# Kernel optimization log

Hardware: AMD Instinct MI355X
Metric: run time of the kernel (lower is better)

The kernel has to match this reference:

```python
import jax, jax.numpy as jnp
import numpy as np

NEG_INF = -jnp.inf


def setup_inputs() -> dict:
    key = jax.random.key(0)
    ks = jax.random.split(key, 8)
    B, Lq, Lk, D, H = 8, 2048, 2048, 256, 128
    queries = jax.random.normal(ks[0], (B, Lq, D), dtype=jnp.float32)
    keys = jax.random.normal(ks[1], (B, Lk, D), dtype=jnp.float32)
    values_1 = jax.random.normal(ks[2], (B, Lk, D), dtype=jnp.float32)
    values_2 = jax.random.normal(ks[3], (B, Lq, D), dtype=jnp.float32)
    values_1_mask = jax.random.randint(ks[4], (B, Lk), 0, 2).astype(bool)
    values_2_mask = jax.random.randint(ks[5], (B, Lq), 0, 2).astype(bool)
    # xavier_normal for Linear(D -> H): std = sqrt(2/(D+H))
    std = float(np.sqrt(2.0 / (D + H)))
    Wq = jax.random.normal(ks[6], (H, D), dtype=jnp.float32) * std
    Wk = jax.random.normal(ks[7], (H, D), dtype=jnp.float32) * std
    scaling = jnp.ones((1, H), dtype=jnp.float32)
    return {
        "queries": queries, "keys": keys,
        "values_1": values_1, "values_1_mask": values_1_mask,
        "values_2": values_2, "values_2_mask": values_2_mask,
        "Wq": Wq, "Wk": Wk, "scaling": scaling,
    }


def reference(queries, keys, values_1, values_1_mask, values_2, values_2_mask, Wq, Wk, scaling):
    # projections + relu (eval mode: dropout inactive)
    pq = jax.nn.relu(jnp.einsum("bqd,hd->bqh", queries, Wq))        # [B,Lq,H]
    pk = jax.nn.relu(jnp.einsum("bkd,hd->bkh", keys, Wk)) * scaling  # [B,Lk,H]
    scores = jnp.einsum("bqh,bkh->bqk", pq, pk)                      # [B,Lq,Lk]

    # branch 2: softmax over queries axis of scores^T, masked by values_2_mask [B,Lq]
    scores_T = jnp.where(values_2_mask[:, None, :], NEG_INF, jnp.swapaxes(scores, 1, 2))  # [B,Lk,Lq]
    alpha_2 = jax.nn.softmax(scores_T, axis=2)
    output_2 = jnp.einsum("bkq,bqd->bkd", alpha_2, values_2)         # [B,Lk,D]

    # branch 1: softmax over keys axis, masked by values_1_mask [B,Lk]
    scores_1 = jnp.where(values_1_mask[:, None, :], NEG_INF, scores)  # [B,Lq,Lk]
    alpha_1 = jax.nn.softmax(scores_1, axis=2)
    output = jnp.einsum("bqk,bkd->bqd", alpha_1, values_1)           # [B,Lq,D]

    return (output, output_2)
```

## Files before the change

### kernel.cpp

```cpp
#include <hip/hip_runtime.h>
#include <cstdint>
#include <math.h>

#define B 8
#define L 2048
#define D 256
#define H 128

typedef __attribute__((ext_vector_type(8))) _Float16 half8;
typedef __attribute__((ext_vector_type(4))) _Float16 half4t;
typedef __attribute__((ext_vector_type(4))) float f32x4;
typedef unsigned short ushort;
typedef unsigned int uint;


__global__ void prep_kernel(const void* __restrict__ raw0,
                            const void* __restrict__ raw1,
                            const float* __restrict__ Wq,
                            const float* __restrict__ Wk,
                            float* __restrict__ fb1,
                            float* __restrict__ fb2,
                            _Float16* __restrict__ Wf) {
    const int t = threadIdx.x;
    const int z = blockIdx.y;
    {
        const void* raw = z ? raw1 : raw0;
        float* outb = z ? fb2 : fb1;
        const uint* wd = (const uint*)raw;
        __shared__ int flag;
        if (t == 0) flag = 0;
        __syncthreads();
        if (wd[t] > 1u) flag = 1;
        __syncthreads();
        const int base = blockIdx.x * 1024;
        if (flag) {
            const uint8_t* by = (const uint8_t*)raw;
#pragma unroll
            for (int j = 0; j < 4; ++j) {
                int i = base + t + 256 * j;
                outb[i] = by[i] ? -INFINITY : 0.f;
            }
        } else {
#pragma unroll
            for (int j = 0; j < 4; ++j) {
                int i = base + t + 256 * j;
                outb[i] = wd[i] ? -INFINITY : 0.f;
            }
        }
    }
    {
        const float* Wsrc = z ? Wk : Wq;
        const int chunk = blockIdx.x * 256 + t;
        const int h = chunk >> 5;
        const int d0 = (chunk & 31) * 8;
        float4 v0 = *(const float4*)(Wsrc + (size_t)h * 256 + d0);
        float4 v1 = *(const float4*)(Wsrc + (size_t)h * 256 + d0 + 4);
        half8 hv;
        hv[0] = (_Float16)v0.x; hv[1] = (_Float16)v0.y;
        hv[2] = (_Float16)v0.z; hv[3] = (_Float16)v0.w;
        hv[4] = (_Float16)v1.x; hv[5] = (_Float16)v1.y;
        hv[6] = (_Float16)v1.z; hv[7] = (_Float16)v1.w;
        const int db = d0 >> 5, dq = (d0 >> 3) & 3;
        size_t off = (size_t)z * 32768 +
                     ((size_t)((h >> 4) * 8 + db)) * 512 + dq * 128 + (h & 15) * 8;
        *(half8*)(Wf + off) = hv;
    }
}

__launch_bounds__(256, 2)
__global__ void proj_mfma_kernel(const float* __restrict__ queries,
                                 const float* __restrict__ keys,
                                 const _Float16* __restrict__ Wf,
                                 const float* __restrict__ scaling,
                                 _Float16* __restrict__ pqo,
                                 _Float16* __restrict__ pko) {
    const int t = threadIdx.x;
    const int w = t >> 6;
    const int lane = t & 63;
    const int l15 = lane & 15;
    const int quad = lane >> 4;
    const int z = blockIdx.z;
    const int half = blockIdx.y;
    const int r0 = blockIdx.x * 64;
    const float* in = z ? keys : queries;
    _Float16* outp = z ? pko : pqo;

    __shared__ __attribute__((aligned(16))) _Float16 Wl[32 * 512];
    __shared__ __attribute__((aligned(16))) _Float16 Af[4][8 * 512];

    {
        const _Float16* wsrc = Wf + ((size_t)z * 64 + half * 32) * 512;
#pragma unroll
        for (int i = 0; i < 8; ++i) {
            const int f = w * 8 + i;
            __builtin_amdgcn_global_load_lds(
                (const __attribute__((address_space(1))) uint*)(wsrc + f * 512 + lane * 8),
                (__attribute__((address_space(3))) uint*)(Wl + f * 512 + lane * 8),
                16, 0, 0);
        }
    }
    {
#pragma unroll
        for (int j = 0; j < 16; ++j) {
            const int idx = t + 256 * j;
            const int row = idx >> 6;
            const int c4 = idx & 63;
            float4 v = *(const float4*)(in + ((size_t)(r0 + row)) * 256 + c4 * 4);
            half4t h4;
            h4[0] = (_Float16)v.x; h4[1] = (_Float16)v.y;
            h4[2] = (_Float16)v.z; h4[3] = (_Float16)v.w;
            const int rt = row >> 4, rl = row & 15;
            const int d0 = c4 * 4;
            const int db = d0 >> 5, dq = (d0 >> 3) & 3, e = d0 & 7;
            *(half4t*)(&Af[rt][db * 512 + dq * 128 + rl * 8 + e]) = h4;
        }
    }
    __syncthreads();

    half8 a[8];
#pragma unroll
    for (int db = 0; db < 8; ++db)
        a[db] = *(const half8*)(&Af[w][db * 512 + lane * 8]);

    f32x4 acc[4];
#pragma unroll
    for (int hti = 0; hti < 4; ++hti) acc[hti] = (f32x4){0.f, 0.f, 0.f, 0.f};
#pragma unroll
    for (int db = 0; db < 8; ++db)
#pragma unroll
        for (int hti = 0; hti < 4; ++hti) {
            half8 bfrag = *(const half8*)(Wl + (hti * 8 + db) * 512 + lane * 8);
            acc[hti] = __builtin_amdgcn_mfma_f32_16x16x32_f16(a[db], bfrag, acc[hti], 0, 0, 0);
        }

    _Float16* S = Af[w];
#pragma unroll
    for (int hti = 0; hti < 4; ++hti) {
        const int hl_ = hti * 16 + l15;
        const int hb = hl_ >> 5, hq = (hl_ >> 3) & 3, e = hl_ & 7;
        const float scl = z ? scaling[half * 64 + hl_] : 1.f;
#pragma unroll
        for (int r = 0; r < 4; ++r) {
            float v = fmaxf(acc[hti][r], 0.f) * scl;
            S[hb * 512 + hq * 128 + (quad * 4 + r) * 8 + e] = (_Float16)v;
        }
    }
    const size_t grow16 = (size_t)(r0 >> 4) + w;
    _Float16* gout = outp + (grow16 * 4 + half * 2) * 512;
#pragma unroll
    for (int hb = 0; hb < 2; ++hb) {
        half8 vv = *(const half8*)(S + hb * 512 + lane * 8);
        *(half8*)(gout + hb * 512 + lane * 8) = vv;
    }
}

__global__ void vtrans_kernel(const float* __restrict__ v1,
                              const float* __restrict__ v2,
                              _Float16* __restrict__ vt1,
                              _Float16* __restrict__ vt2) {
    const int t = threadIdx.x;
    const int zz = blockIdx.z;
    const int b = zz & 7;
    const int which = zz >> 3;
    const float* src = (which ? v2 : v1) + (size_t)b * L * D;
    _Float16* dst = which ? vt2 : vt1;
    const int k0 = blockIdx.x * 64;
    const int d0 = blockIdx.y * 64;
    __shared__ float lt[64][65];
#pragma unroll
    for (int p = 0; p < 4; ++p) {
        int kr = p * 16 + (t >> 4);
        float4 v = *(const float4*)(src + (size_t)(k0 + kr) * D + d0 + (t & 15) * 4);
        lt[(t & 15) * 4 + 0][kr] = v.x;
        lt[(t & 15) * 4 + 1][kr] = v.y;
        lt[(t & 15) * 4 + 2][kr] = v.z;
        lt[(t & 15) * 4 + 3][kr] = v.w;
    }
    __syncthreads();
    const int d = t & 63;
    const int kk = (t >> 6) & 1;
    const int qp = t >> 7;
    const size_t tile = ((size_t)b * L + k0) / 32 + kk;
    const int ct = (d0 + d) >> 4;
    _Float16* base = dst + (tile * 16 + ct) * 512 + (d & 15) * 8;
#pragma unroll
    for (int s = 0; s < 2; ++s) {
        const int qv = qp * 2 + s;
        const float* lr = &lt[d][kk * 32 + qv * 8];
        half8 hv;
#pragma unroll
        for (int e = 0; e < 8; ++e) hv[e] = (_Float16)lr[e];
        *(half8*)(base + qv * 128) = hv;
    }
}

__launch_bounds__(256)
__global__ void score_kernel(const _Float16* __restrict__ pq,
                             const _Float16* __restrict__ pk,
                             const float* __restrict__ fb1,
                             const float* __restrict__ fb2,
                             _Float16* __restrict__ Sb,
                             float* __restrict__ tmax1,
                             float* __restrict__ tmax2,
                             float* __restrict__ mmax) {
    const int t = threadIdx.x;
    const int w = t >> 6;
    const int lane = t & 63;
    const int l15 = lane & 15;
    const int quad = lane >> 4;
    const int bb = blockIdx.z;
    const int k0 = blockIdx.x * 64;
    const int q0 = blockIdx.y * 64;
    const size_t bL = (size_t)bb * L;
    const int qt16 = (q0 >> 4) + w;

    half8 aq[4];
    {
        const _Float16* qb = pq + ((bL + q0 + w * 16) >> 4) * 2048 + lane * 8;
#pragma unroll
        for (int hb = 0; hb < 4; ++hb) aq[hb] = *(const half8*)(qb + hb * 512);
    }

    f32x4 s[4];
#pragma unroll
    for (int jt = 0; jt < 4; ++jt) {
        const _Float16* kb = pk + ((bL + k0 + jt * 16) >> 4) * 2048 + lane * 8;
        f32x4 sv = (f32x4){0.f, 0.f, 0.f, 0.f};
#pragma unroll
        for (int hb = 0; hb < 4; ++hb) {
            half8 bk = *(const half8*)(kb + hb * 512);
            sv = __builtin_amdgcn_mfma_f32_16x16x32_f16(aq[hb], bk, sv, 0, 0, 0);
        }
        s[jt] = sv;
    }

    float b1j[4];
#pragma unroll
    for (int jt = 0; jt < 4; ++jt) b1j[jt] = fb1[bL + k0 + jt * 16 + l15];
    float4 b2v = *(const float4*)(fb2 + bL + q0 + w * 16 + quad * 4);
    float b2r[4] = {b2v.x, b2v.y, b2v.z, b2v.w};

#pragma unroll
    for (int r = 0; r < 4; ++r) {
        float m1 = -INFINITY;
#pragma unroll
        for (int jt = 0; jt < 4; ++jt) m1 = fmaxf(m1, s[jt][r] + b1j[jt]);
        m1 = fmaxf(m1, __shfl_xor(m1, 1));
        m1 = fmaxf(m1, __shfl_xor(m1, 2));
        m1 = fmaxf(m1, __shfl_xor(m1, 4));
        m1 = fmaxf(m1, __shfl_xor(m1, 8));
        if (l15 == 0)
            tmax1[(bL + q0 + w * 16 + quad * 4 + r) * 32 + blockIdx.x] = m1;
    }

#pragma unroll
    for (int jt = 0; jt < 4; ++jt) {
        float m2 = -INFINITY, mm = -INFINITY;
#pragma unroll
        for (int r = 0; r < 4; ++r) {
            m2 = fmaxf(m2, s[jt][r] + b2r[r]);
            mm = fmaxf(mm, s[jt][r]);
        }
        m2 = fmaxf(m2, __shfl_xor(m2, 16));
        m2 = fmaxf(m2, __shfl_xor(m2, 32));
        if (quad == 0)
            tmax2[(bL + k0 + jt * 16 + l15) * 128 + qt16] = m2;
        mm = fmaxf(mm, __shfl_xor(mm, 1));
        mm = fmaxf(mm, __shfl_xor(mm, 2));
        mm = fmaxf(mm, __shfl_xor(mm, 4));
        mm = fmaxf(mm, __shfl_xor(mm, 8));
        mm = fmaxf(mm, __shfl_xor(mm, 16));
        mm = fmaxf(mm, __shfl_xor(mm, 32));
        const size_t mti = ((size_t)bb * 128 + qt16) * 128 + (k0 >> 4) + jt;
        if (lane == 0) mmax[mti] = mm;
        _Float16* sp = Sb + mti * 256 + l15;
#pragma unroll
        for (int r = 0; r < 4; ++r)
            sp[(quad * 4 + r) * 16] = (_Float16)(s[jt][r] - mm);
    }
}

__launch_bounds__(256, 3)
__global__ void attn_pv_kernel(const _Float16* __restrict__ Sb,
                               const float* __restrict__ fb1,
                               const float* __restrict__ fb2,
                               const float* __restrict__ tmax1,
                               const float* __restrict__ tmax2,
                               const float* __restrict__ mmax,
                               const _Float16* __restrict__ vt1,
                               const _Float16* __restrict__ vt2,
                               float* __restrict__ out) {
    const int t = threadIdx.x;
    const int w = t >> 6;
    const int lane = t & 63;
    const int l15 = lane & 15;
    const int quad = lane >> 4;
    const int bb = blockIdx.y;
    const int z = blockIdx.z;
    const int r0 = blockIdx.x * 64;
    const size_t bL = (size_t)bb * L;

    const _Float16* Vp = z ? vt2 : vt1;
    const float* fbb = (z ? fb2 : fb1) + bL;
    float* O = out + (z ? (size_t)B * L * D : 0);

    __shared__ __attribute__((aligned(16))) _Float16 kv[2][16 * 512];
    __shared__ __attribute__((aligned(16))) _Float16 sst[2][4 * 1056];
    __shared__ float mred[64][4];

    {
        const int row = t >> 2, part = t & 3;
        float mv = -INFINITY;
        if (z == 0) {
            const float4* p4 = (const float4*)(tmax1 + ((bL + r0 + row) << 5)) + part * 2;
#pragma unroll
            for (int i = 0; i < 2; ++i) {
                float4 v = p4[i];
                mv = fmaxf(mv, fmaxf(fmaxf(v.x, v.y), fmaxf(v.z, v.w)));
            }
        } else {
            const float4* p4 = (const float4*)(tmax2 + ((bL + r0 + row) << 7)) + part * 8;
#pragma unroll
            for (int i = 0; i < 8; ++i) {
                float4 v = p4[i];
                mv = fmaxf(mv, fmaxf(fmaxf(v.x, v.y), fmaxf(v.z, v.w)));
            }
        }
        mred[row][part] = mv;
    }

    auto stage = [&](int it, int buf) {
        const _Float16* vb = Vp + ((bL + it * 32) >> 5) * (size_t)(16 * 512);
#pragma unroll
        for (int i = 0; i < 4; ++i) {
            const int c = w * 4 + i;
            __builtin_amdgcn_global_load_lds(
                (const __attribute__((address_space(1))) uint*)(vb + c * 512 + lane * 8),
                (__attribute__((address_space(3))) uint*)(&kv[buf][c * 512] + lane * 8),
                16, 0, 0);
        }
        if (z) {
            const _Float16* ssrc = Sb +
                (((size_t)bb * 128 + it * 2 + (w >> 1)) * 128 + (r0 >> 4) + (w & 1) * 2) * 256;
            __builtin_amdgcn_global_load_lds(
                (const __attribute__((address_space(1))) uint*)(ssrc + lane * 8),
                (__attribute__((address_space(3))) uint*)(&sst[buf][w * 1056] + lane * 8),
                16, 0, 0);
        }
    };

    stage(0, 0);
    __syncthreads();

    float mreg;
    {
        const int row = w * 16 + l15;
        mreg = fmaxf(fmaxf(mred[row][0], mred[row][1]),
                     fmaxf(mred[row][2], mred[row][3]));
        mreg = fmaxf(mreg, -1e30f);
    }

    f32x4 acc[16];
#pragma unroll
    for (int ct = 0; ct < 16; ++ct) acc[ct] = (f32x4){0.f, 0.f, 0.f, 0.f};
    float lsum = 0.f;

    for (int it = 0; it < 64; ++it) {
        const int buf = it & 1;
        if (it) __syncthreads();
        if (it + 1 < 64) stage(it + 1, buf ^ 1);

        float c;
        {
            const size_t mmidx = z
                ? (((size_t)bb * 128 + it * 2 + (quad >> 1)) * 128 + (r0 >> 4) + w)
                : (((size_t)bb * 128 + (r0 >> 4) + w) * 128 + it * 2 + (quad >> 1));
            c = mmax[mmidx] - mreg;
        }
        float bj[8];
        {
            const float4* bp = (const float4*)(fbb + it * 32 + quad * 8);
            float4 b0 = bp[0], b1 = bp[1];
            bj[0] = b0.x; bj[1] = b0.y; bj[2] = b0.z; bj[3] = b0.w;
            bj[4] = b1.x; bj[5] = b1.y; bj[6] = b1.z; bj[7] = b1.w;
        }
        float pj[8];
        if (z == 0) {
            const _Float16* sp = Sb +
                (((size_t)bb * 128 + (r0 >> 4) + w) * 128 + it * 2 + (quad >> 1)) * 256 +
                l15 * 16 + (quad & 1) * 8;
            half8 sv = *(const half8*)sp;
#pragma unroll
            for (int j = 0; j < 8; ++j) pj[j] = (float)sv[j];
        } else {
            const _Float16* sl = &sst[buf][((quad >> 1) * 2 + (w >> 1)) * 1056 +
                                           (w & 1) * 256 + l15];
#pragma unroll
            for (int j = 0; j < 8; ++j)
                pj[j] = (float)sl[((quad & 1) * 8 + j) * 16];
        }
        half8 pa;
#pragma unroll
        for (int j = 0; j < 8; ++j) {
            float p = __expf(pj[j] + c + bj[j]);
            pa[j] = (_Float16)p;
            lsum += (float)pa[j];
        }
        const _Float16* kb = kv[buf];
#pragma unroll
        for (int ct = 0; ct < 16; ++ct) {
            half8 bv = *(const half8*)(kb + ct * 512 + lane * 8);
            acc[ct] = __builtin_amdgcn_mfma_f32_16x16x32_f16(pa, bv, acc[ct], 0, 0, 0);
        }
    }

    lsum += __shfl_xor(lsum, 16);
    lsum += __shfl_xor(lsum, 32);
    float inv = (lsum > 0.f) ? (1.f / lsum) : 0.f;

#pragma unroll
    for (int r = 0; r < 4; ++r) {
        const float invr = __shfl(inv, quad * 4 + r);
        float* orow = O + (bL + r0 + w * 16 + quad * 4 + r) * (size_t)D + l15;
#pragma unroll
        for (int ct = 0; ct < 16; ++ct)
            orow[ct * 16] = acc[ct][r] * invr;
    }
}

extern "C" void kernel_launch(void* const* d_in, const int* in_sizes, int n_in,
                              void* d_out, int out_size, void* d_ws, size_t ws_size,
                              hipStream_t stream) {
    const float* queries  = (const float*)d_in[0];
    const float* keys     = (const float*)d_in[1];
    const float* values_1 = (const float*)d_in[2];
    const void*  v1_mask  = d_in[3];
    const float* values_2 = (const float*)d_in[4];
    const void*  v2_mask  = d_in[5];
    const float* Wq       = (const float*)d_in[6];
    const float* Wk       = (const float*)d_in[7];
    const float* scaling  = (const float*)d_in[8];
    float* out = (float*)d_out;

    _Float16* pqw = (_Float16*)d_ws;
    _Float16* pkw = pqw + (size_t)B * L * H;
    _Float16* vt1 = pkw + (size_t)B * L * H;
    _Float16* vt2 = vt1 + (size_t)B * L * D;
    _Float16* Sb  = vt2 + (size_t)B * L * D;
    float* fb1   = (float*)(Sb + (size_t)B * 128 * 128 * 256);
    float* fb2   = fb1 + B * L;
    float* tmax1 = fb2 + B * L;
    float* tmax2 = tmax1 + (size_t)B * L * 32;
    float* mmaxp = tmax2 + (size_t)B * L * 128;
    _Float16* Wf = (_Float16*)(mmaxp + (size_t)B * 128 * 128);

    prep_kernel<<<dim3(16, 2), 256, 0, stream>>>(
        v1_mask, v2_mask, Wq, Wk, fb1, fb2, Wf);
    proj_mfma_kernel<<<dim3(B * L / 64, 2, 2), 256, 0, stream>>>(
        queries, keys, Wf, scaling, pqw, pkw);
    vtrans_kernel<<<dim3(L / 64, D / 64, B * 2), 256, 0, stream>>>(
        values_1, values_2, vt1, vt2);
    score_kernel<<<dim3(L / 64, L / 64, B), 256, 0, stream>>>(
        pqw, pkw, fb1, fb2, Sb, tmax1, tmax2, mmaxp);
    attn_pv_kernel<<<dim3(L / 64, B, 2), 256, 0, stream>>>(
        Sb, fb1, fb2, tmax1, tmax2, mmaxp, vt1, vt2, out);
}
```

Baseline: 243.0 us.

## Triple-buffer PV kernel with LDS staging of scores and prefetched scalars

The PV kernel goes from double to triple buffering of V and score tiles, with two tiles in flight. It now stages the z==0 score tiles into LDS through global_load_lds instead of reading them directly from global memory. It also prefetches the next iteration's row-max and bias values. Barriers and manual vmcnt waits replace __syncthreads so loads can overlap the MFMA work, at the cost of more LDS and occupancy lowered from 3 to 2 blocks per CU.

```diff
diff --git a/kernel.cpp b/kernel.cpp
--- a/kernel.cpp
+++ b/kernel.cpp
@@ -280,7 +280,7 @@
     }
 }
 
-__launch_bounds__(256, 3)
+__launch_bounds__(256, 2)
 __global__ void attn_pv_kernel(const _Float16* __restrict__ Sb,
                                const float* __restrict__ fb1,
                                const float* __restrict__ fb2,
@@ -304,8 +304,8 @@
     const float* fbb = (z ? fb2 : fb1) + bL;
     float* O = out + (z ? (size_t)B * L * D : 0);
 
-    __shared__ __attribute__((aligned(16))) _Float16 kv[2][16 * 512];
-    __shared__ __attribute__((aligned(16))) _Float16 sst[2][4 * 1056];
+    __shared__ __attribute__((aligned(16))) _Float16 kv[3][16 * 512];
+    __shared__ __attribute__((aligned(16))) _Float16 sst[3][4 * 1056];
     __shared__ float mred[64][4];
 
     {
@@ -339,18 +339,33 @@
                 (__attribute__((address_space(3))) uint*)(&kv[buf][c * 512] + lane * 8),
                 16, 0, 0);
         }
-        if (z) {
-            const _Float16* ssrc = Sb +
-                (((size_t)bb * 128 + it * 2 + (w >> 1)) * 128 + (r0 >> 4) + (w & 1) * 2) * 256;
-            __builtin_amdgcn_global_load_lds(
-                (const __attribute__((address_space(1))) uint*)(ssrc + lane * 8),
-                (__attribute__((address_space(3))) uint*)(&sst[buf][w * 1056] + lane * 8),
-                16, 0, 0);
-        }
+        const _Float16* ssrc = z
+            ? Sb + (((size_t)bb * 128 + it * 2 + (w >> 1)) * 128 + (r0 >> 4) + (w & 1) * 2) * 256
+            : Sb + (((size_t)bb * 128 + (r0 >> 4) + w) * 128 + it * 2) * 256;
+        __builtin_amdgcn_global_load_lds(
+            (const __attribute__((address_space(1))) uint*)(ssrc + lane * 8),
+            (__attribute__((address_space(3))) uint*)(&sst[buf][w * 1056] + lane * 8),
+            16, 0, 0);
     };
 
     stage(0, 0);
-    __syncthreads();
+    stage(1, 1);
+    stage(2, 2);
+
+    auto mmidx = [&](int itx) -> size_t {
+        return z ? (((size_t)bb * 128 + itx * 2 + (quad >> 1)) * 128 + (r0 >> 4) + w)
+                 : (((size_t)bb * 128 + (r0 >> 4) + w) * 128 + itx * 2 + (quad >> 1));
+    };
+    float c_cur = mmax[mmidx(0)];
+    float4 b0_cur, b1_cur;
+    {
+        const float4* bp = (const float4*)(fbb + quad * 8);
+        b0_cur = bp[0]; b1_cur = bp[1];
+    }
+
+    asm volatile("s_waitcnt vmcnt(10) lgkmcnt(0)" ::: "memory");
+    __builtin_amdgcn_s_barrier();
+    __builtin_amdgcn_sched_barrier(0);
 
     float mreg;
     {
@@ -365,40 +380,35 @@
     for (int ct = 0; ct < 16; ++ct) acc[ct] = (f32x4){0.f, 0.f, 0.f, 0.f};
     float lsum = 0.f;
 
+    int buf = 0;
     for (int it = 0; it < 64; ++it) {
-        const int buf = it & 1;
-        if (it) __syncthreads();
-        if (it + 1 < 64) stage(it + 1, buf ^ 1);
-
-        float c;
-        {
-            const size_t mmidx = z
-                ? (((size_t)bb * 128 + it * 2 + (quad >> 1)) * 128 + (r0 >> 4) + w)
-                : (((size_t)bb * 128 + (r0 >> 4) + w) * 128 + it * 2 + (quad >> 1));
-            c = mmax[mmidx] - mreg;
-        }
-        float bj[8];
-        {
-            const float4* bp = (const float4*)(fbb + it * 32 + quad * 8);
-            float4 b0 = bp[0], b1 = bp[1];
-            bj[0] = b0.x; bj[1] = b0.y; bj[2] = b0.z; bj[3] = b0.w;
-            bj[4] = b1.x; bj[5] = b1.y; bj[6] = b1.z; bj[7] = b1.w;
-        }
+        float c_nxt = 0.f;
+        float4 b0n = b0_cur, b1n = b1_cur;
+        if (it + 1 < 64) {
+            c_nxt = mmax[mmidx(it + 1)];
+            const float4* bp = (const float4*)(fbb + (it + 1) * 32 + quad * 8);
+            b0n = bp[0]; b1n = bp[1];
+        }
+
         float pj[8];
         if (z == 0) {
-            const _Float16* sp = Sb +
-                (((size_t)bb * 128 + (r0 >> 4) + w) * 128 + it * 2 + (quad >> 1)) * 256 +
-                l15 * 16 + (quad & 1) * 8;
-            half8 sv = *(const half8*)sp;
+            const _Float16* sl =
+                &sst[buf][w * 1056 + (quad >> 1) * 256 + l15 * 16 + (quad & 1) * 8];
+            half8 sv = *(const half8*)sl;
 #pragma unroll
             for (int j = 0; j < 8; ++j) pj[j] = (float)sv[j];
         } else {
-            const _Float16* sl = &sst[buf][((quad >> 1) * 2 + (w >> 1)) * 1056 +
-                                           (w & 1) * 256 + l15];
+            const _Float16* sl =
+                &sst[buf][((quad >> 1) * 2 + (w >> 1)) * 1056 + (w & 1) * 256 + l15];
 #pragma unroll
             for (int j = 0; j < 8; ++j)
                 pj[j] = (float)sl[((quad & 1) * 8 + j) * 16];
         }
+
+        const float c = c_cur - mreg;
+        float bj[8] = {b0_cur.x, b0_cur.y, b0_cur.z, b0_cur.w,
+                       b1_cur.x, b1_cur.y, b1_cur.z, b1_cur.w};
+
         half8 pa;
 #pragma unroll
         for (int j = 0; j < 8; ++j) {
@@ -412,6 +422,24 @@
             half8 bv = *(const half8*)(kb + ct * 512 + lane * 8);
             acc[ct] = __builtin_amdgcn_mfma_f32_16x16x32_f16(pa, bv, acc[ct], 0, 0, 0);
         }
+
+        c_cur = c_nxt; b0_cur = b0n; b1_cur = b1n;
+
+        if (it < 63) {
+            __builtin_amdgcn_s_barrier();
+            __builtin_amdgcn_sched_barrier(0);
+            if (it + 3 < 64) stage(it + 3, buf);
+            if (it < 61)
+                asm volatile("s_waitcnt vmcnt(10)" ::: "memory");
+            else if (it == 61)
+                asm volatile("s_waitcnt vmcnt(5)" ::: "memory");
+            else
+                asm volatile("s_waitcnt vmcnt(0)" ::: "memory");
+            __builtin_amdgcn_sched_barrier(0);
+            __builtin_amdgcn_s_barrier();
+            __builtin_amdgcn_sched_barrier(0);
+        }
+        buf = (buf == 2) ? 0 : buf + 1;
     }
 
     lsum += __shfl_xor(lsum, 16);
```

New measurement: 242.9 us. Within noise of the previous version (-0.1%).

## Deepen PV pipeline with 64-key stages, prefetch-two and vmcnt-controlled barriers

Applied to the files above, without the earlier changes.

Reworks attn_pv_kernel so each pipeline stage covers 64 keys instead of 32, which halves the number of iterations and barriers. Both branches now stage score tiles into LDS, where before branch 1 read them straight from global memory. The kernel prefetches two stages ahead and uses explicit s_waitcnt vmcnt with raw s_barrier instead of __syncthreads, so loads stay in flight across iterations. The row-max reduction moves from an LDS array to wave shuffles. LDS use roughly doubles and launch bounds drop from 3 to 2 blocks per CU, which lowers occupancy in exchange for deeper overlap.

```diff
diff --git a/kernel.cpp b/kernel.cpp
--- a/kernel.cpp
+++ b/kernel.cpp
@@ -280,7 +280,7 @@
     }
 }
 
-__launch_bounds__(256, 3)
+__launch_bounds__(256, 2)
 __global__ void attn_pv_kernel(const _Float16* __restrict__ Sb,
                                const float* __restrict__ fb1,
                                const float* __restrict__ fb2,
@@ -299,118 +299,138 @@
     const int z = blockIdx.z;
     const int r0 = blockIdx.x * 64;
     const size_t bL = (size_t)bb * L;
+    const int qtw = (r0 >> 4) + w;
 
     const _Float16* Vp = z ? vt2 : vt1;
     const float* fbb = (z ? fb2 : fb1) + bL;
     float* O = out + (z ? (size_t)B * L * D : 0);
 
-    __shared__ __attribute__((aligned(16))) _Float16 kv[2][16 * 512];
-    __shared__ __attribute__((aligned(16))) _Float16 sst[2][4 * 1056];
-    __shared__ float mred[64][4];
-
-    {
-        const int row = t >> 2, part = t & 3;
-        float mv = -INFINITY;
-        if (z == 0) {
-            const float4* p4 = (const float4*)(tmax1 + ((bL + r0 + row) << 5)) + part * 2;
-#pragma unroll
-            for (int i = 0; i < 2; ++i) {
-                float4 v = p4[i];
-                mv = fmaxf(mv, fmaxf(fmaxf(v.x, v.y), fmaxf(v.z, v.w)));
-            }
-        } else {
-            const float4* p4 = (const float4*)(tmax2 + ((bL + r0 + row) << 7)) + part * 8;
-#pragma unroll
-            for (int i = 0; i < 8; ++i) {
-                float4 v = p4[i];
-                mv = fmaxf(mv, fmaxf(fmaxf(v.x, v.y), fmaxf(v.z, v.w)));
-            }
-        }
-        mred[row][part] = mv;
-    }
+    __shared__ __attribute__((aligned(16))) _Float16 kv[2][32 * 512];
+    __shared__ __attribute__((aligned(16))) _Float16 sst[2][4096];
 
     auto stage = [&](int it, int buf) {
-        const _Float16* vb = Vp + ((bL + it * 32) >> 5) * (size_t)(16 * 512);
-#pragma unroll
-        for (int i = 0; i < 4; ++i) {
-            const int c = w * 4 + i;
+        const _Float16* vb = Vp + ((bL + (size_t)it * 64) >> 5) * (size_t)(16 * 512);
+#pragma unroll
+        for (int i = 0; i < 8; ++i) {
+            const int c = w * 8 + i;
             __builtin_amdgcn_global_load_lds(
                 (const __attribute__((address_space(1))) uint*)(vb + c * 512 + lane * 8),
                 (__attribute__((address_space(3))) uint*)(&kv[buf][c * 512] + lane * 8),
                 16, 0, 0);
         }
-        if (z) {
-            const _Float16* ssrc = Sb +
-                (((size_t)bb * 128 + it * 2 + (w >> 1)) * 128 + (r0 >> 4) + (w & 1) * 2) * 256;
+#pragma unroll
+        for (int j = 0; j < 2; ++j) {
+            const _Float16* ssrc;
+            if (z == 0) {
+                ssrc = Sb + (((size_t)bb * 128 + qtw) * 128 + it * 4) * 256 +
+                       j * 512 + lane * 8;
+            } else {
+                const int qt = it * 4 + j * 2 + (lane >> 5);
+                ssrc = Sb + (((size_t)bb * 128 + qt) * 128 + qtw) * 256 +
+                       (lane & 31) * 8;
+            }
             __builtin_amdgcn_global_load_lds(
-                (const __attribute__((address_space(1))) uint*)(ssrc + lane * 8),
-                (__attribute__((address_space(3))) uint*)(&sst[buf][w * 1056] + lane * 8),
+                (const __attribute__((address_space(1))) uint*)ssrc,
+                (__attribute__((address_space(3))) uint*)(&sst[buf][w * 1024 + j * 512] + lane * 8),
                 16, 0, 0);
         }
     };
 
     stage(0, 0);
-    __syncthreads();
 
     float mreg;
     {
-        const int row = w * 16 + l15;
-        mreg = fmaxf(fmaxf(mred[row][0], mred[row][1]),
-                     fmaxf(mred[row][2], mred[row][3]));
-        mreg = fmaxf(mreg, -1e30f);
-    }
+        const int row = r0 + w * 16 + l15;
+        float mv = -INFINITY;
+        if (z == 0) {
+            const float4* p4 = (const float4*)(tmax1 + ((bL + row) << 5)) + quad * 2;
+#pragma unroll
+            for (int i = 0; i < 2; ++i) {
+                float4 v = p4[i];
+                mv = fmaxf(mv, fmaxf(fmaxf(v.x, v.y), fmaxf(v.z, v.w)));
+            }
+        } else {
+            const float4* p4 = (const float4*)(tmax2 + ((bL + row) << 7)) + quad * 8;
+#pragma unroll
+            for (int i = 0; i < 8; ++i) {
+                float4 v = p4[i];
+                mv = fmaxf(mv, fmaxf(fmaxf(v.x, v.y), fmaxf(v.z, v.w)));
+            }
+        }
+        mv = fmaxf(mv, __shfl_xor(mv, 16));
+        mv = fmaxf(mv, __shfl_xor(mv, 32));
+        mreg = fmaxf(mv, -1e30f);
+    }
+
+    stage(1, 1);
+
+    asm volatile("s_waitcnt vmcnt(10)" ::: "memory");
+    __builtin_amdgcn_sched_barrier(0);
+    __builtin_amdgcn_s_barrier();
+    __builtin_amdgcn_sched_barrier(0);
 
     f32x4 acc[16];
 #pragma unroll
     for (int ct = 0; ct < 16; ++ct) acc[ct] = (f32x4){0.f, 0.f, 0.f, 0.f};
     float lsum = 0.f;
 
-    for (int it = 0; it < 64; ++it) {
+    for (int it = 0; it < 32; ++it) {
         const int buf = it & 1;
-        if (it) __syncthreads();
-        if (it + 1 < 64) stage(it + 1, buf ^ 1);
-
-        float c;
-        {
-            const size_t mmidx = z
-                ? (((size_t)bb * 128 + it * 2 + (quad >> 1)) * 128 + (r0 >> 4) + w)
-                : (((size_t)bb * 128 + (r0 >> 4) + w) * 128 + it * 2 + (quad >> 1));
-            c = mmax[mmidx] - mreg;
-        }
-        float bj[8];
-        {
-            const float4* bp = (const float4*)(fbb + it * 32 + quad * 8);
-            float4 b0 = bp[0], b1 = bp[1];
-            bj[0] = b0.x; bj[1] = b0.y; bj[2] = b0.z; bj[3] = b0.w;
-            bj[4] = b1.x; bj[5] = b1.y; bj[6] = b1.z; bj[7] = b1.w;
-        }
-        float pj[8];
-        if (z == 0) {
-            const _Float16* sp = Sb +
-                (((size_t)bb * 128 + (r0 >> 4) + w) * 128 + it * 2 + (quad >> 1)) * 256 +
-                l15 * 16 + (quad & 1) * 8;
-            half8 sv = *(const half8*)sp;
-#pragma unroll
-            for (int j = 0; j < 8; ++j) pj[j] = (float)sv[j];
-        } else {
-            const _Float16* sl = &sst[buf][((quad >> 1) * 2 + (w >> 1)) * 1056 +
-                                           (w & 1) * 256 + l15];
-#pragma unroll
-            for (int j = 0; j < 8; ++j)
-                pj[j] = (float)sl[((quad & 1) * 8 + j) * 16];
-        }
-        half8 pa;
-#pragma unroll
-        for (int j = 0; j < 8; ++j) {
-            float p = __expf(pj[j] + c + bj[j]);
-            pa[j] = (_Float16)p;
-            lsum += (float)pa[j];
-        }
-        const _Float16* kb = kv[buf];
-#pragma unroll
-        for (int ct = 0; ct < 16; ++ct) {
-            half8 bv = *(const half8*)(kb + ct * 512 + lane * 8);
-            acc[ct] = __builtin_amdgcn_mfma_f32_16x16x32_f16(pa, bv, acc[ct], 0, 0, 0);
+#pragma unroll
+        for (int jt2 = 0; jt2 < 2; ++jt2) {
+            const int mt = jt2 * 2 + (quad >> 1);
+            float c;
+            if (z == 0)
+                c = mmax[((size_t)bb * 128 + qtw) * 128 + it * 4 + mt] - mreg;
+            else
+                c = mmax[((size_t)bb * 128 + it * 4 + mt) * 128 + qtw] - mreg;
+            float bj[8];
+            {
+                const float4* bp = (const float4*)(fbb + it * 64 + jt2 * 32 + quad * 8);
+                float4 b0 = bp[0], b1 = bp[1];
+                bj[0] = b0.x; bj[1] = b0.y; bj[2] = b0.z; bj[3] = b0.w;
+                bj[4] = b1.x; bj[5] = b1.y; bj[6] = b1.z; bj[7] = b1.w;
+            }
+            float pj[8];
+            if (z == 0) {
+                const _Float16* sl =
+                    &sst[buf][w * 1024 + mt * 256 + l15 * 16 + (quad & 1) * 8];
+                half8 sv = *(const half8*)sl;
+#pragma unroll
+                for (int j = 0; j < 8; ++j) pj[j] = (float)sv[j];
+            } else {
+                const _Float16* sl = &sst[buf][w * 1024 + mt * 256 + l15];
+#pragma unroll
+                for (int j = 0; j < 8; ++j)
+                    pj[j] = (float)sl[((quad & 1) * 8 + j) * 16];
+            }
+            half8 pa;
+#pragma unroll
+            for (int j = 0; j < 8; ++j) {
+                float p = __expf(pj[j] + c + bj[j]);
+                pa[j] = (_Float16)p;
+                lsum += (float)pa[j];
+            }
+            const _Float16* kb = &kv[buf][jt2 * 16 * 512];
+#pragma unroll
+            for (int ct = 0; ct < 16; ++ct) {
+                half8 bv = *(const half8*)(kb + ct * 512 + lane * 8);
+                acc[ct] = __builtin_amdgcn_mfma_f32_16x16x32_f16(pa, bv, acc[ct], 0, 0, 0);
+            }
+        }
+
+        if (it < 31) {
+            __builtin_amdgcn_s_barrier();
+            __builtin_amdgcn_sched_barrier(0);
+            if (it + 2 < 32) {
+                stage(it + 2, buf);
+                asm volatile("s_waitcnt vmcnt(10)" ::: "memory");
+            } else {
+                asm volatile("s_waitcnt vmcnt(0)" ::: "memory");
+            }
+            __builtin_amdgcn_sched_barrier(0);
+            __builtin_amdgcn_s_barrier();
+            __builtin_amdgcn_sched_barrier(0);
         }
     }
 
```

After: 247.5 us. About the same (+1.9%).
